# Kernel optimization log

Hardware: AMD Instinct MI355X
Metric: run time of the kernel (lower is better)

Reference implementation:

```python
import jax, jax.numpy as jnp
import numpy as np

N = 50000
E = 800000
D_IN = 128
D_H = 128
D_OUT = 1


def setup_inputs() -> dict:
    key = jax.random.key(0)
    ks = jax.random.split(key, 12)
    x = jax.random.normal(ks[0], (N, D_IN), dtype=jnp.float32)
    edge_index = jax.random.randint(ks[1], (2, E), 0, N, dtype=jnp.int64)
    def glorot(k, shape):
        lim = float(np.sqrt(6.0 / (shape[0] + shape[1])))
        return jax.random.uniform(k, shape, jnp.float32, -lim, lim)
    return {
        "x": x,
        "edge_index": edge_index,
        "W1": glorot(ks[2], (D_IN, D_H)),  "b1": jnp.zeros((D_H,), jnp.float32),
        "W2": glorot(ks[3], (D_H, D_H)),   "b2": jnp.zeros((D_H,), jnp.float32),
        "W3": glorot(ks[4], (D_H, D_H)),   "b3": jnp.zeros((D_H,), jnp.float32),
        "Wfc": glorot(ks[5], (D_H, D_OUT)), "bfc": jnp.zeros((D_OUT,), jnp.float32),
    }


def _gcn_norm(edge_index, num_nodes):
    # Add self-loops (PyG GCNConv default) and compute symmetric normalization
    loops = jnp.arange(num_nodes, dtype=edge_index.dtype)
    src = jnp.concatenate([edge_index[0], loops])
    dst = jnp.concatenate([edge_index[1], loops])
    ones = jnp.ones(src.shape[0], dtype=jnp.float32)
    deg = jax.ops.segment_sum(ones, dst, num_segments=num_nodes)
    dinv = jnp.where(deg > 0, jax.lax.rsqrt(deg), 0.0)
    norm = dinv[src] * dinv[dst]  # [E + N]
    return src, dst, norm


def _gcn_layer(x, W, b, src, dst, norm, num_nodes):
    xw = x @ W                              # [N, out] dense transform first
    msg = xw[src] * norm[:, None]           # gather + scale
    agg = jax.ops.segment_sum(msg, dst, num_segments=num_nodes)  # scatter-add
    return agg + b


def reference(x, edge_index, W1, b1, W2, b2, W3, b3, Wfc, bfc):
    num_nodes = x.shape[0]
    src, dst, norm = _gcn_norm(edge_index, num_nodes)
    h = jax.nn.relu(_gcn_layer(x, W1, b1, src, dst, norm, num_nodes))
    h = jax.nn.relu(_gcn_layer(h, W2, b2, src, dst, norm, num_nodes))
    h = jax.nn.relu(_gcn_layer(h, W3, b3, src, dst, norm, num_nodes))
    return h @ Wfc + bfc  # [N, 1]
```

## Files before the change

kernel.cpp:

```cpp
#include <hip/hip_runtime.h>

#define D 128
#define SCAN_ELEMS 4096

typedef __attribute__((ext_vector_type(8))) short short8;
typedef __attribute__((ext_vector_type(4))) float f32x4;

__device__ inline void f2bf(float f, short& hi, short& lo) {
    union { float f; unsigned u; } a; a.f = f;
    unsigned r = a.u + 0x7fffu + ((a.u >> 16) & 1u);
    hi = (short)(r >> 16);
    union { unsigned u; float f; } h; h.u = ((unsigned)(unsigned short)hi) << 16;
    union { float f; unsigned u; } b; b.f = f - h.f;
    unsigned r2 = b.u + 0x7fffu + ((b.u >> 16) & 1u);
    lo = (short)(r2 >> 16);
}

__device__ inline unsigned enc24(float f) {
    union { float f; unsigned u; } a; a.f = f;
    unsigned r = a.u + 0x7fu + ((a.u >> 8) & 1u);
    return r >> 8;
}


__device__ void wsplit_body(int tid, const float* __restrict__ W1,
                            const float* __restrict__ W2, const float* __restrict__ W3,
                            short* __restrict__ Bsw) {
    int layer = tid >> 14;
    int rem = tid & 16383;
    int k = rem >> 7, c = rem & 127;
    const float* Wg = (layer == 0) ? W1 : ((layer == 1) ? W2 : W3);
    float v = Wg[k * 128 + c];
    short hi, lo; f2bf(v, hi, lo);
    int ktile = k >> 5, kk = k & 31, q = kk >> 3, j = kk & 7;
    int ct = c >> 4, mm = c & 15, lane = q * 16 + mm;
    int idx = layer * 32768 + ((ktile * 8 + ct) * 64 + lane) * 8 + j;
    Bsw[idx] = hi;
    Bsw[idx + 16384] = lo;
}

__global__ __launch_bounds__(256) void count_wsplit_kernel(const int* __restrict__ dst,
                                                           int* __restrict__ deg,
                                                           unsigned short* __restrict__ rank,
                                                           int e, int nbCount,
                                                           const float* __restrict__ W1,
                                                           const float* __restrict__ W2,
                                                           const float* __restrict__ W3,
                                                           short* __restrict__ Bsw) {
    if ((int)blockIdx.x < nbCount) {
        int i = blockIdx.x * 256 + threadIdx.x;
        if (i < e) rank[i] = (unsigned short)atomicAdd(&deg[dst[i]], 1);
    } else {
        int tid = (blockIdx.x - nbCount) * 256 + threadIdx.x;
        wsplit_body(tid, W1, W2, W3, Bsw);
    }
}

__global__ __launch_bounds__(256) void scan_kernel(const int* __restrict__ deg,
                                                   int* __restrict__ offsets,
                                                   float* __restrict__ dinv, int n) {
    __shared__ int sBase[4];
    __shared__ int waveSums[4];
    int t = threadIdx.x;
    int lane = t & 63, w = t >> 6;

    int lim = blockIdx.x * SCAN_ELEMS;
    int s = 0;
    for (int i = t * 4; i < lim; i += 1024) {
        int4 v = *reinterpret_cast<const int4*>(deg + i);
        s += v.x + v.y + v.z + v.w;
    }
    #pragma unroll
    for (int off = 32; off > 0; off >>= 1) s += __shfl_down(s, off);
    if (lane == 0) sBase[w] = s;

    int base = blockIdx.x * SCAN_ELEMS + t * 16;
    int v[16];
    int ls = 0;
    #pragma unroll
    for (int k = 0; k < 16; ++k) {
        int i = base + k;
        int d = (i < n) ? deg[i] : 0;
        v[k] = d;
        ls += d;
    }
    int incl = ls;
    #pragma unroll
    for (int off = 1; off < 64; off <<= 1) {
        int u = __shfl_up(incl, off);
        if (lane >= off) incl += u;
    }
    if (lane == 63) waveSums[w] = incl;
    __syncthreads();

    int blkBase = sBase[0] + sBase[1] + sBase[2] + sBase[3];
    int waveOff = 0;
    for (int i = 0; i < 4; ++i) if (i < w) waveOff += waveSums[i];
    int off0 = blkBase + waveOff + incl - ls;

    #pragma unroll
    for (int k = 0; k < 16; ++k) {
        int i = base + k;
        if (i < n) {
            offsets[i] = off0;
            dinv[i] = rsqrtf((float)(v[k] + 1));
            off0 += v[k];
        }
    }
}

template<bool SPLIT>
__device__ void gemm_body(int blk, const float* __restrict__ A,
                          const unsigned short* __restrict__ Ah,
                          const unsigned short* __restrict__ Al,
                          const short* __restrict__ Bsw,
                          const float* __restrict__ dinv,
                          unsigned short* __restrict__ xh,
                          unsigned char* __restrict__ xl, int n, int t) {
    int w = t >> 6;
    int lane = t & 63;
    int quad = lane >> 4;
    int m = lane & 15;

    int rowBase = blk * 64 + w * 16;
    int arow = rowBase + m;
    bool valid = arow < n;
    int srow = valid ? arow : 0;

    f32x4 acc[8];
    #pragma unroll
    for (int ct = 0; ct < 8; ++ct) acc[ct] = (f32x4){0.f, 0.f, 0.f, 0.f};

    #pragma unroll
    for (int kt = 0; kt < 4; ++kt) {
        short8 a_hi, a_lo;
        if (SPLIT) {
            size_t off = (size_t)srow * D + kt * 32 + quad * 8;
            a_hi = *reinterpret_cast<const short8*>(Ah + off);
            a_lo = *reinterpret_cast<const short8*>(Al + off);
        } else {
            const float* ap = A + (size_t)srow * D + quad * 8;
            float4 f0 = *reinterpret_cast<const float4*>(ap + kt * 32);
            float4 f1 = *reinterpret_cast<const float4*>(ap + kt * 32 + 4);
            float fv[8] = {f0.x, f0.y, f0.z, f0.w, f1.x, f1.y, f1.z, f1.w};
            #pragma unroll
            for (int j = 0; j < 8; ++j) {
                short h, l; f2bf(valid ? fv[j] : 0.f, h, l);
                a_hi[j] = h; a_lo[j] = l;
            }
        }
        const short* bp = Bsw + (kt * 512 + lane) * 8;
        #pragma unroll
        for (int ct = 0; ct < 8; ++ct) {
            short8 b_hi = *reinterpret_cast<const short8*>(bp + ct * 512);
            short8 b_lo = *reinterpret_cast<const short8*>(bp + 16384 + ct * 512);
            acc[ct] = __builtin_amdgcn_mfma_f32_16x16x32_bf16(a_hi, b_hi, acc[ct], 0, 0, 0);
            acc[ct] = __builtin_amdgcn_mfma_f32_16x16x32_bf16(a_hi, b_lo, acc[ct], 0, 0, 0);
            acc[ct] = __builtin_amdgcn_mfma_f32_16x16x32_bf16(a_lo, b_hi, acc[ct], 0, 0, 0);
        }
    }

    #pragma unroll
    for (int r = 0; r < 4; ++r) {
        int row = rowBase + quad * 4 + r;
        if (row < n) {
            float s = dinv[row];
            size_t rb = (size_t)row * 128 + m;
            #pragma unroll
            for (int ct = 0; ct < 8; ++ct) {
                unsigned e24 = enc24(acc[ct][r] * s);
                xh[rb + ct * 16] = (unsigned short)(e24 >> 8);
                xl[rb + ct * 16] = (unsigned char)(e24 & 0xffu);
            }
        }
    }
}

__global__ __launch_bounds__(256) void gemm_split_kernel(const unsigned short* __restrict__ Ah,
                                                         const unsigned short* __restrict__ Al,
                                                         const short* __restrict__ Bsw,
                                                         const float* __restrict__ dinv,
                                                         unsigned short* __restrict__ xh,
                                                         unsigned char* __restrict__ xl, int n) {
    gemm_body<true>(blockIdx.x, nullptr, Ah, Al, Bsw, dinv, xh, xl, n, threadIdx.x);
}

__global__ __launch_bounds__(256) void fill_gemm_kernel(const int* __restrict__ src,
                                                        const int* __restrict__ dst,
                                                        const int* __restrict__ offsets,
                                                        const unsigned short* __restrict__ rank,
                                                        unsigned short* __restrict__ csr_src,
                                                        int e, int nbFill,
                                                        const float* __restrict__ A,
                                                        const short* __restrict__ Bsw,
                                                        const float* __restrict__ dinv,
                                                        unsigned short* __restrict__ xh,
                                                        unsigned char* __restrict__ xl, int n) {
    if ((int)blockIdx.x < nbFill) {
        int i = blockIdx.x * 256 + threadIdx.x;
        if (i < e) csr_src[offsets[dst[i]] + rank[i]] = (unsigned short)src[i];
    } else {
        gemm_body<false>(blockIdx.x - nbFill, A, nullptr, nullptr, Bsw, dinv, xh, xl, n, threadIdx.x);
    }
}

template<bool FC>
__global__ __launch_bounds__(256) void aggq_kernel(const unsigned short* __restrict__ xh,
                                                   const unsigned char* __restrict__ xl,
                                                   const unsigned short* __restrict__ csr,
                                                   const int* __restrict__ offsets,
                                                   const int* __restrict__ deg,
                                                   const float* __restrict__ dinv,
                                                   const float* __restrict__ bias,
                                                   unsigned short* __restrict__ hh,
                                                   unsigned short* __restrict__ hl,
                                                   const float* __restrict__ fcw,
                                                   const float* __restrict__ fcb,
                                                   float* __restrict__ fcout,
                                                   int n) {
    int wave = (blockIdx.x * blockDim.x + threadIdx.x) >> 6;
    if (wave >= n) return;
    int lane = threadIdx.x & 63;
    int q = lane >> 4;
    int s = lane & 15;
    int node = wave;

    int base = offsets[node];
    int cnt  = deg[node];

    float4 aA0 = make_float4(0.f, 0.f, 0.f, 0.f), aA1 = make_float4(0.f, 0.f, 0.f, 0.f);
    float4 aB0 = make_float4(0.f, 0.f, 0.f, 0.f), aB1 = make_float4(0.f, 0.f, 0.f, 0.f);
    float4 aC0 = make_float4(0.f, 0.f, 0.f, 0.f), aC1 = make_float4(0.f, 0.f, 0.f, 0.f);
    float4 aD0 = make_float4(0.f, 0.f, 0.f, 0.f), aD1 = make_float4(0.f, 0.f, 0.f, 0.f);

    auto gq = [&](int row, float4& x0, float4& x1) {
        const unsigned short* hp = xh + ((size_t)row << 7) + s * 8;
        const unsigned char*  lp = xl + ((size_t)row << 7) + s * 8;
        uint4 h4 = *reinterpret_cast<const uint4*>(hp);
        uint2 l2 = *reinterpret_cast<const uint2*>(lp);
        union { unsigned u; float f; } e0, e1, e2, e3, e4, e5, e6, e7;
        e0.u = __builtin_amdgcn_perm(h4.x, l2.x, 0x0504000Cu);
        e1.u = __builtin_amdgcn_perm(h4.x, l2.x, 0x0706010Cu);
        e2.u = __builtin_amdgcn_perm(h4.y, l2.x, 0x0504020Cu);
        e3.u = __builtin_amdgcn_perm(h4.y, l2.x, 0x0706030Cu);
        e4.u = __builtin_amdgcn_perm(h4.z, l2.y, 0x0504000Cu);
        e5.u = __builtin_amdgcn_perm(h4.z, l2.y, 0x0706010Cu);
        e6.u = __builtin_amdgcn_perm(h4.w, l2.y, 0x0504020Cu);
        e7.u = __builtin_amdgcn_perm(h4.w, l2.y, 0x0706030Cu);
        x0.x += e0.f; x0.y += e1.f; x0.z += e2.f; x0.w += e3.f;
        x1.x += e4.f; x1.y += e5.f; x1.z += e6.f; x1.w += e7.f;
    };

    int total = cnt + 1;
    if (total <= 64) {
        int idx = (lane < cnt) ? (int)csr[base + lane] : node;
        for (int j = 0; j < total; j += 16) {
            int p0 = j + q, p1 = j + 4 + q, p2 = j + 8 + q, p3 = j + 12 + q;
            int s0 = __shfl(idx, p0 & 63);
            int s1 = __shfl(idx, p1 & 63);
            int s2 = __shfl(idx, p2 & 63);
            int s3 = __shfl(idx, p3 & 63);
            if (p0 < total) gq(s0, aA0, aA1);
            if (p1 < total) gq(s1, aB0, aB1);
            if (p2 < total) gq(s2, aC0, aC1);
            if (p3 < total) gq(s3, aD0, aD1);
        }
    } else {
        for (int j = 0; j < cnt; j += 16) {
            int p0 = j + q, p1 = j + 4 + q, p2 = j + 8 + q, p3 = j + 12 + q;
            int s0 = (p0 < cnt) ? (int)csr[base + p0] : 0;
            int s1 = (p1 < cnt) ? (int)csr[base + p1] : 0;
            int s2 = (p2 < cnt) ? (int)csr[base + p2] : 0;
            int s3 = (p3 < cnt) ? (int)csr[base + p3] : 0;
            if (p0 < cnt) gq(s0, aA0, aA1);
            if (p1 < cnt) gq(s1, aB0, aB1);
            if (p2 < cnt) gq(s2, aC0, aC1);
            if (p3 < cnt) gq(s3, aD0, aD1);
        }
        if (q == 0) gq(node, aA0, aA1);
    }

    aA0.x += aB0.x + aC0.x + aD0.x;
    aA0.y += aB0.y + aC0.y + aD0.y;
    aA0.z += aB0.z + aC0.z + aD0.z;
    aA0.w += aB0.w + aC0.w + aD0.w;
    aA1.x += aB1.x + aC1.x + aD1.x;
    aA1.y += aB1.y + aC1.y + aD1.y;
    aA1.z += aB1.z + aC1.z + aD1.z;
    aA1.w += aB1.w + aC1.w + aD1.w;
    #pragma unroll
    for (int off = 16; off < 64; off <<= 1) {
        aA0.x += __shfl_xor(aA0.x, off);
        aA0.y += __shfl_xor(aA0.y, off);
        aA0.z += __shfl_xor(aA0.z, off);
        aA0.w += __shfl_xor(aA0.w, off);
        aA1.x += __shfl_xor(aA1.x, off);
        aA1.y += __shfl_xor(aA1.y, off);
        aA1.z += __shfl_xor(aA1.z, off);
        aA1.w += __shfl_xor(aA1.w, off);
    }

    float di = dinv[node];
    float4 b0 = *reinterpret_cast<const float4*>(bias + s * 8);
    float4 b1 = *reinterpret_cast<const float4*>(bias + s * 8 + 4);
    float r0 = fmaxf(di * aA0.x + b0.x, 0.f);
    float r1 = fmaxf(di * aA0.y + b0.y, 0.f);
    float r2 = fmaxf(di * aA0.z + b0.z, 0.f);
    float r3 = fmaxf(di * aA0.w + b0.w, 0.f);
    float r4 = fmaxf(di * aA1.x + b1.x, 0.f);
    float r5 = fmaxf(di * aA1.y + b1.y, 0.f);
    float r6 = fmaxf(di * aA1.z + b1.z, 0.f);
    float r7 = fmaxf(di * aA1.w + b1.w, 0.f);

    if (FC) {
        float4 w0 = *reinterpret_cast<const float4*>(fcw + s * 8);
        float4 w1 = *reinterpret_cast<const float4*>(fcw + s * 8 + 4);
        float p = r0 * w0.x + r1 * w0.y + r2 * w0.z + r3 * w0.w
                + r4 * w1.x + r5 * w1.y + r6 * w1.z + r7 * w1.w;
        p += __shfl_xor(p, 1);
        p += __shfl_xor(p, 2);
        p += __shfl_xor(p, 4);
        p += __shfl_xor(p, 8);
        if (lane == 0) fcout[node] = p + fcb[0];
    } else if (q == 0) {
        short8 sh, sl;
        float rv[8] = {r0, r1, r2, r3, r4, r5, r6, r7};
        #pragma unroll
        for (int i = 0; i < 8; ++i) {
            short h, l; f2bf(rv[i], h, l);
            sh[i] = h; sl[i] = l;
        }
        size_t off = (size_t)node * D + s * 8;
        *reinterpret_cast<short8*>(hh + off) = sh;
        *reinterpret_cast<short8*>(hl + off) = sl;
    }
}


extern "C" void kernel_launch(void* const* d_in, const int* in_sizes, int n_in,
                              void* d_out, int out_size, void* d_ws, size_t ws_size,
                              hipStream_t stream) {
    const float* x   = (const float*)d_in[0];
    const int*   ei  = (const int*)d_in[1];
    const float* W1  = (const float*)d_in[2];
    const float* b1  = (const float*)d_in[3];
    const float* W2  = (const float*)d_in[4];
    const float* b2  = (const float*)d_in[5];
    const float* W3  = (const float*)d_in[6];
    const float* b3  = (const float*)d_in[7];
    const float* Wfc = (const float*)d_in[8];
    const float* bfc = (const float*)d_in[9];
    float* outp = (float*)d_out;

    const int n = in_sizes[0] / D;
    const int e = in_sizes[1] / 2;
    const int* src = ei;
    const int* dst = ei + e;

    char* ws = (char*)d_ws;
    size_t off = 0;
    auto alloc = [&](size_t bytes) {
        void* p = ws + off;
        off += (bytes + 255) & ~(size_t)255;
        return p;
    };
    int*            deg     = (int*)alloc((size_t)n * 4);
    size_t          zero_bytes = off;
    int*            offsets = (int*)alloc((size_t)n * 4);
    float*          dinv    = (float*)alloc((size_t)n * 4);
    short*          Bsw     = (short*)alloc((size_t)3 * 32768 * 2);
    unsigned short* rank    = (unsigned short*)alloc((size_t)e * 2);
    unsigned short* csr_src = (unsigned short*)alloc((size_t)e * 2);
    unsigned short* xhbuf   = (unsigned short*)alloc((size_t)n * 128 * 2);
    unsigned char*  xlbuf   = (unsigned char*)alloc((size_t)n * 128);
    unsigned short* hhbuf   = (unsigned short*)alloc((size_t)n * 128 * 2);
    unsigned short* hlbuf   = (unsigned short*)alloc((size_t)n * 128 * 2);

    int eb256 = (e + 255) / 256;
    int scan_blocks = (n + SCAN_ELEMS - 1) / SCAN_ELEMS;
    int gemm_blocks = (n + 63) / 64;
    int agg_blocks  = (n + 3) / 4;

    hipMemsetAsync(ws, 0, zero_bytes, stream);
    count_wsplit_kernel<<<eb256 + 192, 256, 0, stream>>>(dst, deg, rank, e, eb256,
                                                         W1, W2, W3, Bsw);
    scan_kernel<<<scan_blocks, 256, 0, stream>>>(deg, offsets, dinv, n);
    fill_gemm_kernel<<<eb256 + gemm_blocks, 256, 0, stream>>>(src, dst, offsets, rank, csr_src,
                                                              e, eb256, x, Bsw, dinv,
                                                              xhbuf, xlbuf, n);
    aggq_kernel<false><<<agg_blocks, 256, 0, stream>>>(xhbuf, xlbuf, csr_src, offsets, deg, dinv,
                                                       b1, hhbuf, hlbuf, nullptr, nullptr, nullptr, n);
    gemm_split_kernel<<<gemm_blocks, 256, 0, stream>>>(hhbuf, hlbuf, Bsw + 32768, dinv,
                                                       xhbuf, xlbuf, n);
    aggq_kernel<false><<<agg_blocks, 256, 0, stream>>>(xhbuf, xlbuf, csr_src, offsets, deg, dinv,
                                                       b2, hhbuf, hlbuf, nullptr, nullptr, nullptr, n);
    gemm_split_kernel<<<gemm_blocks, 256, 0, stream>>>(hhbuf, hlbuf, Bsw + 65536, dinv,
                                                       xhbuf, xlbuf, n);
    aggq_kernel<true><<<agg_blocks, 256, 0, stream>>>(xhbuf, xlbuf, csr_src, offsets, deg, dinv,
                                                      b3, nullptr, nullptr, Wfc, bfc, outp, n);
}
```

Baseline: 330.7 us.

## Split aggregation feature dimension across four blocks per node group

The aggregation kernel now launches four blocks per group of four nodes, each handling a 32-column slice of the 128 features. Within a wave, 16 edge slots are processed in parallel, with 4 lanes per row covering 8 columns each, instead of 4 edge slots times 16 lanes. The final FC projection becomes a partial dot product per chunk, accumulated with atomicAdd into an output that the scan kernel pre-initialises with the FC bias. The aim is more parallelism and memory-level concurrency per node, at the cost of redundant index loads, four times as many blocks, and atomics on the output.

```diff
diff --git a/kernel.cpp b/kernel.cpp
--- a/kernel.cpp
+++ b/kernel.cpp
@@ -58,7 +58,9 @@
 
 __global__ __launch_bounds__(256) void scan_kernel(const int* __restrict__ deg,
                                                    int* __restrict__ offsets,
-                                                   float* __restrict__ dinv, int n) {
+                                                   float* __restrict__ dinv, int n,
+                                                   float* __restrict__ fcout,
+                                                   const float* __restrict__ fcb) {
     __shared__ int sBase[4];
     __shared__ int waveSums[4];
     int t = threadIdx.x;
@@ -98,12 +100,14 @@
     for (int i = 0; i < 4; ++i) if (i < w) waveOff += waveSums[i];
     int off0 = blkBase + waveOff + incl - ls;
 
+    float b0 = fcb[0];
     #pragma unroll
     for (int k = 0; k < 16; ++k) {
         int i = base + k;
         if (i < n) {
             offsets[i] = off0;
             dinv[i] = rsqrtf((float)(v[k] + 1));
+            fcout[i] = b0;
             off0 += v[k];
         }
     }
@@ -215,27 +219,27 @@
                                                    unsigned short* __restrict__ hh,
                                                    unsigned short* __restrict__ hl,
                                                    const float* __restrict__ fcw,
-                                                   const float* __restrict__ fcb,
                                                    float* __restrict__ fcout,
                                                    int n) {
-    int wave = (blockIdx.x * blockDim.x + threadIdx.x) >> 6;
-    if (wave >= n) return;
+    int blk = blockIdx.x;
+    int chunk = blk & 3;
+    int wv = threadIdx.x >> 6;
+    int node = (blk >> 2) * 4 + wv;
+    if (node >= n) return;
     int lane = threadIdx.x & 63;
-    int q = lane >> 4;
-    int s = lane & 15;
-    int node = wave;
+    int q = lane >> 2;
+    int s = lane & 3;
+    int cb = chunk * 32 + s * 8;
 
     int base = offsets[node];
     int cnt  = deg[node];
 
     float4 aA0 = make_float4(0.f, 0.f, 0.f, 0.f), aA1 = make_float4(0.f, 0.f, 0.f, 0.f);
     float4 aB0 = make_float4(0.f, 0.f, 0.f, 0.f), aB1 = make_float4(0.f, 0.f, 0.f, 0.f);
-    float4 aC0 = make_float4(0.f, 0.f, 0.f, 0.f), aC1 = make_float4(0.f, 0.f, 0.f, 0.f);
-    float4 aD0 = make_float4(0.f, 0.f, 0.f, 0.f), aD1 = make_float4(0.f, 0.f, 0.f, 0.f);
 
     auto gq = [&](int row, float4& x0, float4& x1) {
-        const unsigned short* hp = xh + ((size_t)row << 7) + s * 8;
-        const unsigned char*  lp = xl + ((size_t)row << 7) + s * 8;
+        const unsigned short* hp = xh + ((size_t)row << 7) + cb;
+        const unsigned char*  lp = xl + ((size_t)row << 7) + cb;
         uint4 h4 = *reinterpret_cast<const uint4*>(hp);
         uint2 l2 = *reinterpret_cast<const uint2*>(lp);
         union { unsigned u; float f; } e0, e1, e2, e3, e4, e5, e6, e7;
@@ -254,42 +258,28 @@
     int total = cnt + 1;
     if (total <= 64) {
         int idx = (lane < cnt) ? (int)csr[base + lane] : node;
-        for (int j = 0; j < total; j += 16) {
-            int p0 = j + q, p1 = j + 4 + q, p2 = j + 8 + q, p3 = j + 12 + q;
+        for (int j = 0; j < total; j += 32) {
+            int p0 = j + q, p1 = j + 16 + q;
             int s0 = __shfl(idx, p0 & 63);
             int s1 = __shfl(idx, p1 & 63);
-            int s2 = __shfl(idx, p2 & 63);
-            int s3 = __shfl(idx, p3 & 63);
             if (p0 < total) gq(s0, aA0, aA1);
             if (p1 < total) gq(s1, aB0, aB1);
-            if (p2 < total) gq(s2, aC0, aC1);
-            if (p3 < total) gq(s3, aD0, aD1);
         }
     } else {
-        for (int j = 0; j < cnt; j += 16) {
-            int p0 = j + q, p1 = j + 4 + q, p2 = j + 8 + q, p3 = j + 12 + q;
+        for (int j = 0; j < cnt; j += 32) {
+            int p0 = j + q, p1 = j + 16 + q;
             int s0 = (p0 < cnt) ? (int)csr[base + p0] : 0;
             int s1 = (p1 < cnt) ? (int)csr[base + p1] : 0;
-            int s2 = (p2 < cnt) ? (int)csr[base + p2] : 0;
-            int s3 = (p3 < cnt) ? (int)csr[base + p3] : 0;
             if (p0 < cnt) gq(s0, aA0, aA1);
             if (p1 < cnt) gq(s1, aB0, aB1);
-            if (p2 < cnt) gq(s2, aC0, aC1);
-            if (p3 < cnt) gq(s3, aD0, aD1);
         }
         if (q == 0) gq(node, aA0, aA1);
     }
 
-    aA0.x += aB0.x + aC0.x + aD0.x;
-    aA0.y += aB0.y + aC0.y + aD0.y;
-    aA0.z += aB0.z + aC0.z + aD0.z;
-    aA0.w += aB0.w + aC0.w + aD0.w;
-    aA1.x += aB1.x + aC1.x + aD1.x;
-    aA1.y += aB1.y + aC1.y + aD1.y;
-    aA1.z += aB1.z + aC1.z + aD1.z;
-    aA1.w += aB1.w + aC1.w + aD1.w;
-    #pragma unroll
-    for (int off = 16; off < 64; off <<= 1) {
+    aA0.x += aB0.x; aA0.y += aB0.y; aA0.z += aB0.z; aA0.w += aB0.w;
+    aA1.x += aB1.x; aA1.y += aB1.y; aA1.z += aB1.z; aA1.w += aB1.w;
+    #pragma unroll
+    for (int off = 4; off < 64; off <<= 1) {
         aA0.x += __shfl_xor(aA0.x, off);
         aA0.y += __shfl_xor(aA0.y, off);
         aA0.z += __shfl_xor(aA0.z, off);
@@ -301,8 +291,8 @@
     }
 
     float di = dinv[node];
-    float4 b0 = *reinterpret_cast<const float4*>(bias + s * 8);
-    float4 b1 = *reinterpret_cast<const float4*>(bias + s * 8 + 4);
+    float4 b0 = *reinterpret_cast<const float4*>(bias + cb);
+    float4 b1 = *reinterpret_cast<const float4*>(bias + cb + 4);
     float r0 = fmaxf(di * aA0.x + b0.x, 0.f);
     float r1 = fmaxf(di * aA0.y + b0.y, 0.f);
     float r2 = fmaxf(di * aA0.z + b0.z, 0.f);
@@ -313,15 +303,13 @@
     float r7 = fmaxf(di * aA1.w + b1.w, 0.f);
 
     if (FC) {
-        float4 w0 = *reinterpret_cast<const float4*>(fcw + s * 8);
-        float4 w1 = *reinterpret_cast<const float4*>(fcw + s * 8 + 4);
+        float4 w0 = *reinterpret_cast<const float4*>(fcw + cb);
+        float4 w1 = *reinterpret_cast<const float4*>(fcw + cb + 4);
         float p = r0 * w0.x + r1 * w0.y + r2 * w0.z + r3 * w0.w
                 + r4 * w1.x + r5 * w1.y + r6 * w1.z + r7 * w1.w;
         p += __shfl_xor(p, 1);
         p += __shfl_xor(p, 2);
-        p += __shfl_xor(p, 4);
-        p += __shfl_xor(p, 8);
-        if (lane == 0) fcout[node] = p + fcb[0];
+        if (lane == 0) atomicAdd(fcout + node, p);
     } else if (q == 0) {
         short8 sh, sl;
         float rv[8] = {r0, r1, r2, r3, r4, r5, r6, r7};
@@ -330,7 +318,7 @@
             short h, l; f2bf(rv[i], h, l);
             sh[i] = h; sl[i] = l;
         }
-        size_t off = (size_t)node * D + s * 8;
+        size_t off = (size_t)node * D + cb;
         *reinterpret_cast<short8*>(hh + off) = sh;
         *reinterpret_cast<short8*>(hl + off) = sl;
     }
@@ -379,23 +367,23 @@
     int eb256 = (e + 255) / 256;
     int scan_blocks = (n + SCAN_ELEMS - 1) / SCAN_ELEMS;
     int gemm_blocks = (n + 63) / 64;
-    int agg_blocks  = (n + 3) / 4;
+    int agg_blocks  = ((n + 3) / 4) * 4;
 
     hipMemsetAsync(ws, 0, zero_bytes, stream);
     count_wsplit_kernel<<<eb256 + 192, 256, 0, stream>>>(dst, deg, rank, e, eb256,
                                                          W1, W2, W3, Bsw);
-    scan_kernel<<<scan_blocks, 256, 0, stream>>>(deg, offsets, dinv, n);
+    scan_kernel<<<scan_blocks, 256, 0, stream>>>(deg, offsets, dinv, n, outp, bfc);
     fill_gemm_kernel<<<eb256 + gemm_blocks, 256, 0, stream>>>(src, dst, offsets, rank, csr_src,
                                                               e, eb256, x, Bsw, dinv,
                                                               xhbuf, xlbuf, n);
     aggq_kernel<false><<<agg_blocks, 256, 0, stream>>>(xhbuf, xlbuf, csr_src, offsets, deg, dinv,
-                                                       b1, hhbuf, hlbuf, nullptr, nullptr, nullptr, n);
+                                                       b1, hhbuf, hlbuf, nullptr, nullptr, n);
     gemm_split_kernel<<<gemm_blocks, 256, 0, stream>>>(hhbuf, hlbuf, Bsw + 32768, dinv,
                                                        xhbuf, xlbuf, n);
     aggq_kernel<false><<<agg_blocks, 256, 0, stream>>>(xhbuf, xlbuf, csr_src, offsets, deg, dinv,
-                                                       b2, hhbuf, hlbuf, nullptr, nullptr, nullptr, n);
+                                                       b2, hhbuf, hlbuf, nullptr, nullptr, n);
     gemm_split_kernel<<<gemm_blocks, 256, 0, stream>>>(hhbuf, hlbuf, Bsw + 65536, dinv,
                                                        xhbuf, xlbuf, n);
     aggq_kernel<true><<<agg_blocks, 256, 0, stream>>>(xhbuf, xlbuf, csr_src, offsets, deg, dinv,
-                                                      b3, nullptr, nullptr, Wfc, bfc, outp, n);
-}
+                                                      b3, nullptr, nullptr, Wfc, outp, n);
+}
```

New measurement: 490.5 us. 1.48x slower.
